# Performance work log

Measured on AMD Instinct MI355X. Metric: run time of the kernel, lower is better.

Reference implementation:

```python
import jax, jax.numpy as jnp
import numpy as np

D_K = 64


def setup_inputs() -> dict:
    key = jax.random.key(0)
    kq, kk, kv = jax.random.split(key, 3)
    B, H, S, D = 2, 16, 2048, D_K
    Q = jax.random.normal(kq, (B, H, S, D), dtype=jnp.float32)
    K = jax.random.normal(kk, (B, H, S, D), dtype=jnp.float32)
    V = jax.random.normal(kv, (B, H, S, D), dtype=jnp.float32)
    # causal mask: True = masked out (matches torch masked_fill_ semantics)
    causal = ~jnp.tril(jnp.ones((S, S), dtype=bool))
    attn_mask = jnp.broadcast_to(causal, (B, 1, S, S))
    return {"Q": Q, "K": K, "V": V, "attn_mask": attn_mask}


def reference(Q, K, V, attn_mask):
    # scores = Q K^T / sqrt(d_k), masked positions -> -1e9, softmax, then A V
    scale = 1.0 / np.sqrt(D_K).astype(np.float32)
    scores = jnp.einsum("bhqd,bhkd->bhqk", Q, K) * scale
    scores = jnp.where(attn_mask, jnp.float32(-1e9), scores)
    attn = jax.nn.softmax(scores, axis=-1)
    context = jnp.einsum("bhqk,bhkd->bhqd", attn, V)
    return (context, attn)
```

## Files before the change

kernel.cpp:

```cpp
#include <hip/hip_runtime.h>

typedef _Float16 half8  __attribute__((ext_vector_type(8)));
typedef _Float16 half4v __attribute__((ext_vector_type(4)));
typedef float    f32x4  __attribute__((ext_vector_type(4)));

#define S_LEN  2048
#define D_HEAD 64
#define TQ     16
#define EBS    2056

static __device__ __forceinline__ half8 cvt8(float4 a, float4 b) {
    half8 h;
    h[0] = (_Float16)a.x; h[1] = (_Float16)a.y; h[2] = (_Float16)a.z; h[3] = (_Float16)a.w;
    h[4] = (_Float16)b.x; h[5] = (_Float16)b.y; h[6] = (_Float16)b.z; h[7] = (_Float16)b.w;
    return h;
}

static __device__ __forceinline__ f32x4 attn_seg(const _Float16* er, int kb, int qg, float il) {
    f32x4 o;
    if (kb > qg) { o[0] = o[1] = o[2] = o[3] = 0.0f; return o; }
    half4v e = *(const half4v*)(er + kb);
    if (kb + 3 <= qg) {
        o[0] = (float)e[0] * il; o[1] = (float)e[1] * il;
        o[2] = (float)e[2] * il; o[3] = (float)e[3] * il;
    } else {
        o[0] = (float)e[0] * il;
        o[1] = (kb + 1 <= qg) ? (float)e[1] * il : 0.0f;
        o[2] = (kb + 2 <= qg) ? (float)e[2] * il : 0.0f;
        o[3] = (kb + 3 <= qg) ? (float)e[3] * il : 0.0f;
    }
    return o;
}

__global__ void prep_kv(const float* __restrict__ K, _Float16* __restrict__ Kh,
                        const float* __restrict__ V, _Float16* __restrict__ Vt) {
    __shared__ _Float16 lt[D_HEAD][136];
    const int bh = blockIdx.y;
    const int k0 = blockIdx.x * 128;
    const int t  = threadIdx.x;
    {
        const size_t b8 = ((size_t)bh * S_LEN + k0) * D_HEAD / 8;
#pragma unroll
        for (int j = 0; j < 4; ++j) {
            const size_t i = b8 + t + j * 256;
            const float4* p = (const float4*)K + i * 2;
            ((half8*)Kh)[i] = cvt8(p[0], p[1]);
        }
    }
    {
        const int kk = t >> 1, hf = t & 1;
        const float* vp = V + (size_t)bh * S_LEN * D_HEAD + (size_t)(k0 + kk) * D_HEAD + hf * 32;
#pragma unroll
        for (int j = 0; j < 8; ++j) {
            float4 a = *(const float4*)(vp + j * 4);
            lt[hf * 32 + j * 4 + 0][kk] = (_Float16)a.x;
            lt[hf * 32 + j * 4 + 1][kk] = (_Float16)a.y;
            lt[hf * 32 + j * 4 + 2][kk] = (_Float16)a.z;
            lt[hf * 32 + j * 4 + 3][kk] = (_Float16)a.w;
        }
    }
    __syncthreads();
    {
        const int d = t >> 2, kq = t & 3;
        _Float16* dst = Vt + ((size_t)bh * D_HEAD + d) * S_LEN + k0 + kq * 32;
        const half8* src = (const half8*)&lt[d][kq * 32];
#pragma unroll
        for (int j = 0; j < 4; ++j) ((half8*)dst)[j] = src[j];
    }
}

template <bool USE_WS>
__global__ __launch_bounds__(512, 4)
void sdpa_main(const float* __restrict__ Q, const float* __restrict__ K,
               const _Float16* __restrict__ Kh, const float* __restrict__ V,
               const _Float16* __restrict__ Vt, float* __restrict__ ctx,
               float* __restrict__ attn) {
    __shared__ __align__(16) _Float16 ebuf[TQ][EBS];
    __shared__ float rowsum[TQ];
    __shared__ __align__(16) float pbuf[4][64][4];

    const int tid  = threadIdx.x;
    const int wave = tid >> 6;
    const int lane = tid & 63;
    const int c    = lane & 15;
    const int quad = lane >> 4;
    const int dg   = wave & 3;
    const int wg   = wave >> 2;

    int qt, bh;
    if (gridDim.y == 1) {
        const int f = blockIdx.x;
        bh = ((f & 7) << 2) | ((f >> 3) & 3);
        qt = 127 - (f >> 5);
    } else {
        qt = blockIdx.x;
        bh = blockIdx.y;
    }

    const int q0 = qt * TQ;
    const int n_k   = q0 + TQ;
    const int n_t16 = n_k >> 4;
    const int n_c32 = (n_k + 31) >> 5;

    const size_t base = (size_t)bh * (S_LEN * D_HEAD);

    if (tid < TQ) rowsum[tid] = 0.0f;
    if ((n_k & 31) && tid < 256) {
        int r = tid >> 4, kk = n_k + (tid & 15);
        ebuf[r][kk] = (_Float16)0.0f;
    }

    half8 qf0, qf1;
    {
        const float* qp = Q + base + (size_t)(q0 + c) * D_HEAD + quad * 8;
        qf0 = cvt8(*(const float4*)qp, *(const float4*)(qp + 4));
        qf1 = cvt8(*(const float4*)(qp + 32), *(const float4*)(qp + 36));
    }
    __syncthreads();

    float psum = 0.0f;
    for (int t = wave; t < n_t16; t += 8) {
        const int k0 = t * 16;
        half8 kf0, kf1;
        if (USE_WS) {
            const _Float16* kp = Kh + base + (size_t)(k0 + c) * D_HEAD + quad * 8;
            kf0 = *(const half8*)kp;
            kf1 = *(const half8*)(kp + 32);
        } else {
            const float* kp = K + base + (size_t)(k0 + c) * D_HEAD + quad * 8;
            kf0 = cvt8(*(const float4*)kp, *(const float4*)(kp + 4));
            kf1 = cvt8(*(const float4*)(kp + 32), *(const float4*)(kp + 36));
        }
        f32x4 s = {0.0f, 0.0f, 0.0f, 0.0f};
        s = __builtin_amdgcn_mfma_f32_16x16x32_f16(kf0, qf0, s, 0, 0, 0);
        s = __builtin_amdgcn_mfma_f32_16x16x32_f16(kf1, qf1, s, 0, 0, 0);

        half4v ev;
#pragma unroll
        for (int r = 0; r < 4; ++r) {
            const int kg = k0 + quad * 4 + r;
            float e = (kg <= q0 + c) ? __expf(s[r] * 0.125f) : 0.0f;
            psum += e;
            ev[r] = (_Float16)e;
        }
        *(half4v*)&ebuf[c][k0 + quad * 4] = ev;
    }
    psum += __shfl_xor(psum, 16);
    psum += __shfl_xor(psum, 32);
    if (lane < 16) atomicAdd(&rowsum[c], psum);
    __syncthreads();

    f32x4 cacc = {0.0f, 0.0f, 0.0f, 0.0f};
    {
        const int r  = tid >> 5;
        const int c4 = (tid & 31) * 4;
        const int qg = q0 + r;
        const float il = 1.0f / rowsum[r];
        const _Float16* er = ebuf[r];
        float* rowp = attn + (size_t)bh * S_LEN * S_LEN + (size_t)qg * S_LEN;
        const _Float16* vb = USE_WS
            ? Vt + ((size_t)bh * D_HEAD + dg * 16 + c) * S_LEN
            : nullptr;

        int chk = wg;
#pragma unroll
        for (int it = 0; it < 8; ++it) {
            const int lim = ((it + 1) * n_c32) >> 3;
            for (; chk < lim; chk += 2) {
                const int k0 = chk * 32;
                half8 af = *(const half8*)&ebuf[c][k0 + quad * 8];
                half8 bf;
                if (USE_WS) {
                    bf = *(const half8*)(vb + k0 + quad * 8);
                } else {
#pragma unroll
                    for (int j = 0; j < 8; ++j)
                        bf[j] = (_Float16)V[base + (size_t)(k0 + quad * 8 + j) * D_HEAD + dg * 16 + c];
                }
                cacc = __builtin_amdgcn_mfma_f32_16x16x32_f16(af, bf, cacc, 0, 0, 0);
            }
            const int colA = it * 256 + c4;
            const int colB = colA + 128;
            f32x4 oA = attn_seg(er, colA, qg, il);
            f32x4 oB = attn_seg(er, colB, qg, il);
            *(f32x4*)(rowp + colA) = oA;
            *(f32x4*)(rowp + colB) = oB;
        }
    }

    if (wg == 1) *(f32x4*)&pbuf[dg][lane][0] = cacc;
    __syncthreads();
    if (wg == 0) {
        const f32x4 pp = *(const f32x4*)&pbuf[dg][lane][0];
#pragma unroll
        for (int rr = 0; rr < 4; ++rr) {
            const int qr = quad * 4 + rr;
            ctx[base + (size_t)(q0 + qr) * D_HEAD + dg * 16 + c] =
                (cacc[rr] + pp[rr]) * (1.0f / rowsum[qr]);
        }
    }
}

extern "C" void kernel_launch(void* const* d_in, const int* in_sizes, int n_in,
                              void* d_out, int out_size, void* d_ws, size_t ws_size,
                              hipStream_t stream) {
    const float* Q = (const float*)d_in[0];
    const float* K = (const float*)d_in[1];
    const float* V = (const float*)d_in[2];

    const int BH = in_sizes[0] / (S_LEN * D_HEAD);
    float* ctx  = (float*)d_out;
    float* attn = (float*)d_out + (size_t)in_sizes[0];

    const size_t nKV  = (size_t)in_sizes[1];
    const size_t need = 2 * nKV * sizeof(_Float16);

    if (ws_size >= need) {
        _Float16* Kh = (_Float16*)d_ws;
        _Float16* Vt = Kh + nKV;
        prep_kv<<<dim3(S_LEN / 128, BH), 256, 0, stream>>>(K, Kh, V, Vt);
        if (BH == 32) {
            sdpa_main<true><<<dim3((S_LEN / TQ) * BH, 1), 512, 0, stream>>>(Q, K, Kh, V, Vt, ctx, attn);
        } else {
            sdpa_main<true><<<dim3(S_LEN / TQ, BH), 512, 0, stream>>>(Q, K, Kh, V, Vt, ctx, attn);
        }
    } else {
        sdpa_main<false><<<dim3(S_LEN / TQ, BH), 512, 0, stream>>>(Q, K, nullptr, V, nullptr, ctx, attn);
    }
}
```

Baseline: 677.8 us.

## Split zero-fill of masked attention tiles into separate kernel, separate PV loop

Adds a zfill kernel that writes zeros to the upper-triangular 128-column blocks of the attention matrix up front. The main kernel then stores only column segments at or below the diagonal. The PV MFMA loop is pulled out of the interleaved store loop into its own pass. The intent is to take the bulk zero-store traffic off the long-tail main-kernel blocks and run it as a cheap streaming kernel. The cost is an extra launch, and the PV/store overlap from the interleaving is lost.

```diff
diff --git a/kernel.cpp b/kernel.cpp
--- a/kernel.cpp
+++ b/kernel.cpp
@@ -32,6 +32,19 @@
     return o;
 }
 
+__global__ void zfill(float* __restrict__ attn) {
+    const int s = blockIdx.y + 1;
+    const int j = blockIdx.x;
+    if (j * 32 >= s * 128) return;
+    const int bh = blockIdx.z;
+    const int r  = j * 32 + (threadIdx.x >> 3);
+    float* p = attn + ((size_t)bh * S_LEN + r) * S_LEN + s * 128 + (threadIdx.x & 7) * 4;
+    f32x4 z = {0.0f, 0.0f, 0.0f, 0.0f};
+#pragma unroll
+    for (int k = 0; k < 4; ++k)
+        *(f32x4*)(p + k * 32) = z;
+}
+
 __global__ void prep_kv(const float* __restrict__ K, _Float16* __restrict__ Kh,
                         const float* __restrict__ V, _Float16* __restrict__ Vt) {
     __shared__ _Float16 lt[D_HEAD][136];
@@ -152,39 +165,43 @@
 
     f32x4 cacc = {0.0f, 0.0f, 0.0f, 0.0f};
     {
+        const _Float16* vb = USE_WS
+            ? Vt + ((size_t)bh * D_HEAD + dg * 16 + c) * S_LEN
+            : nullptr;
+        for (int chk = wg; chk < n_c32; chk += 2) {
+            const int k0 = chk * 32;
+            half8 af = *(const half8*)&ebuf[c][k0 + quad * 8];
+            half8 bf;
+            if (USE_WS) {
+                bf = *(const half8*)(vb + k0 + quad * 8);
+            } else {
+#pragma unroll
+                for (int j = 0; j < 8; ++j)
+                    bf[j] = (_Float16)V[base + (size_t)(k0 + quad * 8 + j) * D_HEAD + dg * 16 + c];
+            }
+            cacc = __builtin_amdgcn_mfma_f32_16x16x32_f16(af, bf, cacc, 0, 0, 0);
+        }
+    }
+
+    {
         const int r  = tid >> 5;
         const int c4 = (tid & 31) * 4;
         const int qg = q0 + r;
         const float il = 1.0f / rowsum[r];
         const _Float16* er = ebuf[r];
         float* rowp = attn + (size_t)bh * S_LEN * S_LEN + (size_t)qg * S_LEN;
-        const _Float16* vb = USE_WS
-            ? Vt + ((size_t)bh * D_HEAD + dg * 16 + c) * S_LEN
-            : nullptr;
-
-        int chk = wg;
-#pragma unroll
-        for (int it = 0; it < 8; ++it) {
-            const int lim = ((it + 1) * n_c32) >> 3;
-            for (; chk < lim; chk += 2) {
-                const int k0 = chk * 32;
-                half8 af = *(const half8*)&ebuf[c][k0 + quad * 8];
-                half8 bf;
-                if (USE_WS) {
-                    bf = *(const half8*)(vb + k0 + quad * 8);
-                } else {
-#pragma unroll
-                    for (int j = 0; j < 8; ++j)
-                        bf[j] = (_Float16)V[base + (size_t)(k0 + quad * 8 + j) * D_HEAD + dg * 16 + c];
-                }
-                cacc = __builtin_amdgcn_mfma_f32_16x16x32_f16(af, bf, cacc, 0, 0, 0);
+        const int itend = ((q0 + TQ - 1) >> 8) + 1;
+        for (int it = 0; it < itend; ++it) {
+            const int sA = it * 256;
+            const int colA = sA + c4;
+            if (sA <= qg) {
+                f32x4 oA = attn_seg(er, colA, qg, il);
+                *(f32x4*)(rowp + colA) = oA;
             }
-            const int colA = it * 256 + c4;
-            const int colB = colA + 128;
-            f32x4 oA = attn_seg(er, colA, qg, il);
-            f32x4 oB = attn_seg(er, colB, qg, il);
-            *(f32x4*)(rowp + colA) = oA;
-            *(f32x4*)(rowp + colB) = oB;
+            if (sA + 128 <= qg) {
+                f32x4 oB = attn_seg(er, colA + 128, qg, il);
+                *(f32x4*)(rowp + colA + 128) = oB;
+            }
         }
     }
 
@@ -214,6 +231,8 @@
 
     const size_t nKV  = (size_t)in_sizes[1];
     const size_t need = 2 * nKV * sizeof(_Float16);
+
+    if (BH == 32) zfill<<<dim3(60, 15, 32), 256, 0, stream>>>(attn);
 
     if (ws_size >= need) {
         _Float16* Kh = (_Float16*)d_ws;
```

Result: slower. 721.3 us (+6.4%).
